# Kernel tuning notes

Measured on AMD Instinct MI355X. Metric: run time of the kernel, lower is better.

## Reference

```python
import jax, jax.numpy as jnp
import numpy as np

IN_FEATURES = 4096
OUT_FEATURES = 16384
TOKENS = 32


def setup_inputs() -> dict:
    key = jax.random.key(0)
    k1, k2, k3, k4 = jax.random.split(key, 4)
    x = jax.random.normal(k1, (TOKENS, IN_FEATURES), dtype=jnp.float16)
    # int8-valued weights in [-127, 127]
    weight_int8 = jax.random.randint(k2, (OUT_FEATURES, IN_FEATURES), -127, 128, dtype=jnp.int32)
    # per-output-channel scale, positive (amax/127 in the original)
    scale = (jax.random.uniform(k3, (OUT_FEATURES,), dtype=jnp.float32) * 0.02 + 1e-4).astype(jnp.float16)
    bias = jax.random.normal(k4, (OUT_FEATURES,), dtype=jnp.float16)
    return {"x": x, "weight_int8": weight_int8, "scale": scale, "bias": bias}


def reference(x, weight_int8, scale, bias):
    # Dequantize int8 weights to compute dtype with per-row scale, then linear.
    w = weight_int8.astype(jnp.float16) * scale[:, None]          # [out, in] fp16
    return jnp.dot(x, w.T) + bias                                  # [tokens, out]
```

## Files before the change

### kernel.cpp

```cpp
#include <hip/hip_runtime.h>
#include <hip/hip_bf16.h>


typedef __attribute__((ext_vector_type(4))) int    i32x4;
typedef __attribute__((ext_vector_type(4))) float  f32x4;
typedef __attribute__((ext_vector_type(8))) short  s16x8;
typedef __attribute__((ext_vector_type(8))) __bf16 bf16x8;

constexpr int K = 4096;
constexpr int N = 16384;
constexpr int BKI = 1024;
constexpr int NT = K / BKI;
constexpr int PITCH = 4096 + 16;
constexpr size_t XB_OFF = 0;

__device__ inline unsigned short f2bf_rne(float f) {
    unsigned u = __builtin_bit_cast(unsigned, f);
    u += 0x7FFF + ((u >> 16) & 1);
    return (unsigned short)(u >> 16);
}

__device__ inline bf16x8 cvtW(i32x4 lo, i32x4 hi) {
    s16x8 r;
#pragma unroll
    for (int i = 0; i < 4; ++i) {
        r[i]     = (short)(__builtin_bit_cast(unsigned, (float)lo[i]) >> 16);
        r[i + 4] = (short)(__builtin_bit_cast(unsigned, (float)hi[i]) >> 16);
    }
    return __builtin_bit_cast(bf16x8, r);
}

__global__ __launch_bounds__(256) void xcvt_kernel(const float* __restrict__ x,
                                                   unsigned short* __restrict__ xb) {
    const int i = (blockIdx.x * 256 + threadIdx.x) * 8;
    f32x4 lo = *reinterpret_cast<const f32x4*>(x + i);
    f32x4 hi = *reinterpret_cast<const f32x4*>(x + i + 4);
    s16x8 r;
#pragma unroll
    for (int j = 0; j < 4; ++j) {
        r[j]     = (short)f2bf_rne(lo[j]);
        r[j + 4] = (short)f2bf_rne(hi[j]);
    }
    *reinterpret_cast<s16x8*>(xb + i) = r;
}

__global__ __launch_bounds__(256, 2) void w8gemm_kernel(
    const __bf16* __restrict__ xb,
    const int* __restrict__ w,
    const float* __restrict__ scale,
    const float* __restrict__ bias,
    float* __restrict__ out)
{
    extern __shared__ char smem[];

    const int tid  = threadIdx.x;
    const int lane = tid & 63;
    const int wave = tid >> 6;
    const int n16  = lane & 15;
    const int quad = lane >> 4;

    const int c0 = blockIdx.x * 16;

    auto stage = [&](int it) {
#pragma unroll
        for (int j = 0; j < 4; ++j) {
            const int row = wave * 4 + j;
            const char* gsrc = (const char*)(w + (size_t)(c0 + row) * K + it * BKI)
                               + (size_t)lane * 16;
            char* ldst = smem + row * PITCH + lane * 16;
#pragma unroll
            for (int s = 0; s < 4; ++s) {
                __builtin_amdgcn_global_load_lds(
                    (const __attribute__((address_space(1))) void*)(gsrc + s * 1024),
                    (__attribute__((address_space(3))) void*)(ldst + s * 1024),
                    16, 0, 2 );
            }
        }
    };

    const char* lrow = smem + n16 * PITCH + quad * 32 + wave * 1024;
    const __bf16* __restrict__ xr0 = xb + (size_t)n16 * K + wave * 256 + quad * 8;
    const __bf16* __restrict__ xr1 = xr0 + (size_t)16 * K;

    f32x4 acc0 = {0.f, 0.f, 0.f, 0.f};
    f32x4 acc1 = {0.f, 0.f, 0.f, 0.f};

    stage(0);
#pragma unroll 1
    for (int it = 0; it < NT; ++it) {
        bf16x8 aX0[8], aX1[8];
#pragma unroll
        for (int j = 0; j < 8; ++j) {
            const int off = it * BKI + j * 32;
            aX0[j] = *reinterpret_cast<const bf16x8*>(xr0 + off);
            aX1[j] = *reinterpret_cast<const bf16x8*>(xr1 + off);
        }
        __syncthreads();
#pragma unroll
        for (int j = 0; j < 8; ++j) {
            i32x4 b0 = *reinterpret_cast<const i32x4*>(lrow + j * 128);
            i32x4 b1 = *reinterpret_cast<const i32x4*>(lrow + j * 128 + 16);
            bf16x8 bf = cvtW(b0, b1);
            acc0 = __builtin_amdgcn_mfma_f32_16x16x32_bf16(aX0[j], bf, acc0, 0, 0, 0);
            acc1 = __builtin_amdgcn_mfma_f32_16x16x32_bf16(aX1[j], bf, acc1, 0, 0, 0);
        }
        __syncthreads();
        if (it + 1 < NT) stage(it + 1);
    }

    __syncthreads();
    float* red = (float*)smem;
#pragma unroll
    for (int v = 0; v < 4; ++v) {
        red[wave * 512 + lane * 8 + v]     = acc0[v];
        red[wave * 512 + lane * 8 + 4 + v] = acc1[v];
    }
    __syncthreads();
#pragma unroll
    for (int pp = 0; pp < 2; ++pp) {
        const int p = tid + pp * 256;
        float s = red[p] + red[512 + p] + red[1024 + p] + red[1536 + p];
        const int pl   = p >> 3;
        const int r    = p & 7;
        const int half = r >> 2;
        const int v    = r & 3;
        const int pn   = pl & 15;
        const int pq   = pl >> 4;
        const int token = half * 16 + pq * 4 + v;
        const int c = c0 + pn;
        out[(size_t)token * N + c] = s * scale[c] + bias[c];
    }
}

extern "C" void kernel_launch(void* const* d_in, const int* in_sizes, int n_in,
                              void* d_out, int out_size, void* d_ws, size_t ws_size,
                              hipStream_t stream) {
    const float* x     = (const float*)d_in[0];
    const int*   w     = (const int*)d_in[1];
    const float* scale = (const float*)d_in[2];
    const float* bias  = (const float*)d_in[3];
    float* out = (float*)d_out;

    unsigned short* xb = (unsigned short*)((char*)d_ws + XB_OFF);

    xcvt_kernel<<<dim3(64), dim3(256), 0, stream>>>(x, xb);
    w8gemm_kernel<<<dim3(N / 16), dim3(256), 16 * PITCH, stream>>>(
        (const __bf16*)xb, w, scale, bias, out);
}
```

Before: 368.0 us.

## Load int32 weights directly to registers with double-buffered fragments, dropping LDS staging

Replaces the LDS staging of weight tiles through global_load_lds, along with its barrier-synchronised loop, with direct per-lane global loads into register fragments. Two register buffers of four k-steps each are software-pipelined so the next chunk's loads are issued while the current one is converted and fed to MFMA. Each wave now owns a contiguous 1024-wide K slice instead of an interleaved slice. The change removes the LDS round-trip and barriers but uses more registers and relies on the memory system to hide global latency without a deep prefetch.

Measured after the change: 378.9 us. 3.0% more time.

```diff
diff --git a/kernel.cpp b/kernel.cpp
--- a/kernel.cpp
+++ b/kernel.cpp
@@ -9,9 +9,6 @@
 
 constexpr int K = 4096;
 constexpr int N = 16384;
-constexpr int BKI = 1024;
-constexpr int NT = K / BKI;
-constexpr int PITCH = 4096 + 16;
 constexpr size_t XB_OFF = 0;
 
 __device__ inline unsigned short f2bf_rne(float f) {
@@ -51,7 +48,7 @@
     const float* __restrict__ bias,
     float* __restrict__ out)
 {
-    extern __shared__ char smem[];
+    __shared__ float red[2048];
 
     const int tid  = threadIdx.x;
     const int lane = tid & 63;
@@ -61,55 +58,54 @@
 
     const int c0 = blockIdx.x * 16;
 
-    auto stage = [&](int it) {
-#pragma unroll
-        for (int j = 0; j < 4; ++j) {
-            const int row = wave * 4 + j;
-            const char* gsrc = (const char*)(w + (size_t)(c0 + row) * K + it * BKI)
-                               + (size_t)lane * 16;
-            char* ldst = smem + row * PITCH + lane * 16;
-#pragma unroll
-            for (int s = 0; s < 4; ++s) {
-                __builtin_amdgcn_global_load_lds(
-                    (const __attribute__((address_space(1))) void*)(gsrc + s * 1024),
-                    (__attribute__((address_space(3))) void*)(ldst + s * 1024),
-                    16, 0, 2 );
-            }
-        }
-    };
-
-    const char* lrow = smem + n16 * PITCH + quad * 32 + wave * 1024;
-    const __bf16* __restrict__ xr0 = xb + (size_t)n16 * K + wave * 256 + quad * 8;
-    const __bf16* __restrict__ xr1 = xr0 + (size_t)16 * K;
+    const i32x4* __restrict__ wp =
+        reinterpret_cast<const i32x4*>(w + (size_t)(c0 + n16) * K
+                                         + wave * 1024 + quad * 8);
+    const bf16x8* __restrict__ xp0 =
+        reinterpret_cast<const bf16x8*>(xb + (size_t)n16 * K
+                                           + wave * 1024 + quad * 8);
+    const bf16x8* __restrict__ xp1 =
+        reinterpret_cast<const bf16x8*>(xb + (size_t)(n16 + 16) * K
+                                           + wave * 1024 + quad * 8);
 
     f32x4 acc0 = {0.f, 0.f, 0.f, 0.f};
     f32x4 acc1 = {0.f, 0.f, 0.f, 0.f};
 
-    stage(0);
-#pragma unroll 1
-    for (int it = 0; it < NT; ++it) {
-        bf16x8 aX0[8], aX1[8];
+    struct Frag { i32x4 b0, b1; bf16x8 x0, x1; };
+    Frag A[4], B[4];
+
+    auto loadC = [&](Frag (&f)[4], int c) {
 #pragma unroll
-        for (int j = 0; j < 8; ++j) {
-            const int off = it * BKI + j * 32;
-            aX0[j] = *reinterpret_cast<const bf16x8*>(xr0 + off);
-            aX1[j] = *reinterpret_cast<const bf16x8*>(xr1 + off);
+        for (int j = 0; j < 4; ++j) {
+            const int s = c * 4 + j;
+            f[j].b0 = wp[s * 8];
+            f[j].b1 = wp[s * 8 + 1];
+            f[j].x0 = xp0[s * 4];
+            f[j].x1 = xp1[s * 4];
         }
-        __syncthreads();
+    };
+    auto compC = [&](Frag (&f)[4]) {
 #pragma unroll
-        for (int j = 0; j < 8; ++j) {
-            i32x4 b0 = *reinterpret_cast<const i32x4*>(lrow + j * 128);
-            i32x4 b1 = *reinterpret_cast<const i32x4*>(lrow + j * 128 + 16);
-            bf16x8 bf = cvtW(b0, b1);
-            acc0 = __builtin_amdgcn_mfma_f32_16x16x32_bf16(aX0[j], bf, acc0, 0, 0, 0);
-            acc1 = __builtin_amdgcn_mfma_f32_16x16x32_bf16(aX1[j], bf, acc1, 0, 0, 0);
+        for (int j = 0; j < 4; ++j) {
+            bf16x8 bf = cvtW(f[j].b0, f[j].b1);
+            acc0 = __builtin_amdgcn_mfma_f32_16x16x32_bf16(f[j].x0, bf, acc0, 0, 0, 0);
+            acc1 = __builtin_amdgcn_mfma_f32_16x16x32_bf16(f[j].x1, bf, acc1, 0, 0, 0);
         }
-        __syncthreads();
-        if (it + 1 < NT) stage(it + 1);
+    };
+
+    loadC(A, 0);
+    loadC(B, 1);
+#pragma unroll
+    for (int cp = 0; cp < 8; ++cp) {
+        if ((cp & 1) == 0) {
+            compC(A);
+            if (cp + 2 < 8) loadC(A, cp + 2);
+        } else {
+            compC(B);
+            if (cp + 2 < 8) loadC(B, cp + 2);
+        }
     }
 
-    __syncthreads();
-    float* red = (float*)smem;
 #pragma unroll
     for (int v = 0; v < 4; ++v) {
         red[wave * 512 + lane * 8 + v]     = acc0[v];
@@ -144,6 +140,6 @@
     unsigned short* xb = (unsigned short*)((char*)d_ws + XB_OFF);
 
     xcvt_kernel<<<dim3(64), dim3(256), 0, stream>>>(x, xb);
-    w8gemm_kernel<<<dim3(N / 16), dim3(256), 16 * PITCH, stream>>>(
+    w8gemm_kernel<<<dim3(N / 16), dim3(256), 0, stream>>>(
         (const __bf16*)xb, w, scale, bias, out);
 }
```
